# Kernel optimization log

Measured on AMD Instinct MI355X. Metric: run time of the kernel, lower is better.

Reference implementation:

```python
import jax, jax.numpy as jnp
import numpy as np

N, E = 20000, 640000
LATENT, HID, OUT, HEADS = 512, 256, 128, 2
NEG_SLOPE = 0.2


def setup_inputs() -> dict:
    key = jax.random.key(0)
    ks = jax.random.split(key, 12)
    s = 0.02
    return {
        "z": jax.random.normal(ks[0], (N, LATENT), dtype=jnp.float32),
        "edge_index": jax.random.randint(ks[1], (2, E), 0, N, dtype=jnp.int64),
        "W1": jax.random.normal(ks[2], (LATENT, HID), dtype=jnp.float32) * s,
        "b1": jnp.zeros((HID,), dtype=jnp.float32),
        "W2": jax.random.normal(ks[3], (HID, HID * HEADS), dtype=jnp.float32) * s,
        "b2": jnp.zeros((HID * HEADS,), dtype=jnp.float32),
        "Wg": jax.random.normal(ks[4], (HID * HEADS, HEADS * OUT), dtype=jnp.float32) * s,
        "att_src": jax.random.normal(ks[5], (HEADS, OUT), dtype=jnp.float32) * s,
        "att_dst": jax.random.normal(ks[6], (HEADS, OUT), dtype=jnp.float32) * s,
        "bias_g": jnp.zeros((HEADS * OUT,), dtype=jnp.float32),
        "W3": jax.random.normal(ks[7], (OUT * HEADS, 512), dtype=jnp.float32) * s,
        "b3": jnp.zeros((512,), dtype=jnp.float32),
    }


def _gat_conv(x, edge_index, Wg, att_src, att_dst, bias_g):
    n = x.shape[0]
    # add self loops (PyG GATConv default add_self_loops=True)
    loops = jnp.tile(jnp.arange(n, dtype=edge_index.dtype)[None, :], (2, 1))
    ei = jnp.concatenate([edge_index, loops], axis=1)
    src, dst = ei[0], ei[1]
    xp = (x @ Wg).reshape(n, HEADS, OUT)          # [N,H,C]
    a_src = jnp.einsum('nhc,hc->nh', xp, att_src)  # [N,H]
    a_dst = jnp.einsum('nhc,hc->nh', xp, att_dst)
    alpha = jax.nn.leaky_relu(a_src[src] + a_dst[dst], NEG_SLOPE)  # [E+N,H]
    amax = jax.ops.segment_max(alpha, dst, num_segments=n)
    alpha = jnp.exp(alpha - amax[dst])
    denom = jax.ops.segment_sum(alpha, dst, num_segments=n)
    alpha = alpha / jnp.maximum(denom[dst], 1e-16)
    msg = xp[src] * alpha[:, :, None]              # [E+N,H,C]
    out = jax.ops.segment_sum(msg, dst, num_segments=n)  # [N,H,C]
    return out.reshape(n, HEADS * OUT) + bias_g


def reference(z, edge_index, W1, b1, W2, b2, Wg, att_src, att_dst, bias_g, W3, b3):
    x = jax.nn.relu(z @ W1 + b1)
    x = jax.nn.relu(x @ W2 + b2)
    x = _gat_conv(x, edge_index, Wg, att_src, att_dst, bias_g)
    return x @ W3 + b3
```

## Files before the change

### kernel.cpp

```cpp
#include <hip/hip_runtime.h>
#include <hip/hip_bf16.h>
#include <float.h>

#define N_NODES 20000
#define LATENT  512
#define HID     256
#define OUT_C   128
#define HEADS   2
#define HC      256
#define NEG_SLOPE 0.2f

typedef _Float16 half8 __attribute__((ext_vector_type(8)));
typedef __attribute__((ext_vector_type(4))) float f32x4;

__device__ __forceinline__ ushort f2h(float v) {
    _Float16 h = (_Float16)v;
    return *(ushort*)&h;
}
__device__ __forceinline__ float h2f(ushort u) {
    _Float16 h = *(_Float16*)&u;
    return (float)h;
}

__device__ __forceinline__ void gl_lds16(const ushort* g, ushort* l) {
    __builtin_amdgcn_global_load_lds(
        (const __attribute__((address_space(1))) unsigned int*)g,
        (__attribute__((address_space(3))) unsigned int*)l, 16, 0, 0);
}

template<int BN>
__global__ __launch_bounds__(256) void gemm_f16(
    const ushort* __restrict__ A, const ushort* __restrict__ BT,
    const float* __restrict__ bias,
    float* __restrict__ Cf, ushort* __restrict__ Ch,
    int M, int N, int K, int relu)
{
    constexpr int NI  = BN / 32;
    constexpr int BUF = 4096 + BN * 32;
    __shared__ ushort lds[2 * BUF];
    ushort* buf0 = lds;
    ushort* buf1 = lds + BUF;

    const int t = threadIdx.x;
    const int l = t & 63;
    const int w = t >> 6;
    const int wm = (w >> 1) * 64;
    const int wn = (w & 1) * (BN / 2);
    const int lm = l & 15;
    const int q  = l >> 4;
    const int q4 = q * 4;

    const int row0 = blockIdx.x * 128;
    const int col0 = blockIdx.y * BN;

    const int jr0 = w * 16 + (l >> 2);
    const int gsh = (((l & 3) ^ ((l >> 4) & 3)) << 3);
    const ushort* gA0 = A + (size_t)(row0 + jr0) * K + gsh;
    const ushort* gA1 = gA0 + (size_t)64 * K;
    const ushort* gB0 = BT + (size_t)(col0 + jr0) * K + gsh;
    const ushort* gB1 = gB0 + (size_t)64 * K;
    const int dA0 = w * 512, dA1 = (4 + w) * 512;
    const int dB0 = 4096 + w * 512, dB1 = 4096 + (4 + w) * 512;

    const int csw = ((q ^ ((lm >> 2) & 3)) << 3);

    const f32x4 zf = {0.f, 0.f, 0.f, 0.f};
    f32x4 acc[4][NI];
    #pragma unroll
    for (int i = 0; i < 4; ++i)
        #pragma unroll
        for (int j = 0; j < NI; ++j) acc[i][j] = zf;

    auto issue = [&](int kk, ushort* B) {
        gl_lds16(gA0 + kk, B + dA0);
        gl_lds16(gA1 + kk, B + dA1);
        gl_lds16(gB0 + kk, B + dB0);
        if (BN == 128) gl_lds16(gB1 + kk, B + dB1);
    };

    auto compute = [&](const ushort* B) {
        half8 bf[NI];
        #pragma unroll
        for (int ni = 0; ni < NI; ++ni) {
            const int boff = (wn + ni * 16 + lm) * 32 + csw;
            bf[ni] = *(const half8*)&B[4096 + boff];
        }
        #pragma unroll
        for (int mi = 0; mi < 4; ++mi) {
            const int aoff = (wm + mi * 16 + lm) * 32 + csw;
            half8 af = *(const half8*)&B[aoff];
            #pragma unroll
            for (int ni = 0; ni < NI; ++ni)
                acc[mi][ni] = __builtin_amdgcn_mfma_f32_16x16x32_f16(
                    af, bf[ni], acc[mi][ni], 0, 0, 0);
        }
    };

    issue(0, buf0);
    __syncthreads();
    for (int k0 = 0; k0 < K; k0 += 64) {
        issue(k0 + 32, buf1);
        compute(buf0);
        __syncthreads();
        if (k0 + 64 < K) issue(k0 + 64, buf0);
        compute(buf1);
        __syncthreads();
    }

    #pragma unroll
    for (int mi = 0; mi < 4; ++mi) {
        #pragma unroll
        for (int ni = 0; ni < NI; ++ni) {
            const int col = col0 + wn + ni * 16 + lm;
            const float bv = bias ? bias[col] : 0.f;
            #pragma unroll
            for (int r = 0; r < 4; ++r) {
                const int row = row0 + wm + mi * 16 + q4 + r;
                if (row >= M) continue;
                float v = acc[mi][ni][r] + bv;
                if (relu) v = fmaxf(v, 0.f);
                const size_t idx = (size_t)row * N + col;
                if (Cf) Cf[idx] = v;
                if (Ch) Ch[idx] = f2h(v);
            }
        }
    }
}

__global__ __launch_bounds__(256) void cvt_kernel(
    const float* __restrict__ x, ushort* __restrict__ o, int n4)
{
    int i = blockIdx.x * 256 + threadIdx.x;
    if (i >= n4) return;
    float4 v = ((const float4*)x)[i];
    ((ushort4*)o)[i] = make_ushort4(f2h(v.x), f2h(v.y), f2h(v.z), f2h(v.w));
}

__global__ __launch_bounds__(256) void transpose_cvt_kernel(
    const float* __restrict__ W, ushort* __restrict__ T, int K, int N)
{
    int i = blockIdx.x * 256 + threadIdx.x;
    if (i >= K * N) return;
    int k = i / N, n = i - k * N;
    T[(size_t)n * K + k] = f2h(W[i]);
}

__global__ __launch_bounds__(256) void att_kernel(
    const ushort* __restrict__ xp, const float* __restrict__ att_src,
    const float* __restrict__ att_dst,
    float* __restrict__ a_src, float* __restrict__ a_dst, int n)
{
    int gw = (blockIdx.x * blockDim.x + threadIdx.x) >> 6;
    int lane = threadIdx.x & 63;
    if (gw >= 2 * n) return;
    int node = gw >> 1, h = gw & 1;
    const ushort* row = xp + (size_t)node * HC + h * OUT_C;
    const float* as = att_src + h * OUT_C;
    const float* ad = att_dst + h * OUT_C;
    float r0 = h2f(row[lane]), r1 = h2f(row[lane + 64]);
    float s1 = r0 * as[lane] + r1 * as[lane + 64];
    float s2 = r0 * ad[lane] + r1 * ad[lane + 64];
    #pragma unroll
    for (int off = 32; off > 0; off >>= 1) {
        s1 += __shfl_down(s1, off);
        s2 += __shfl_down(s2, off);
    }
    if (lane == 0) { a_src[gw] = s1; a_dst[gw] = s2; }
}

__global__ void zero_int2(int* deg, int* cursor, int n)
{
    int i = blockIdx.x * blockDim.x + threadIdx.x;
    if (i < n) { deg[i] = 0; cursor[i] = 0; }
}

__global__ __launch_bounds__(256) void hist_kernel(
    const int* __restrict__ dst, int* deg, int E_real, int ET)
{
    int e = blockIdx.x * blockDim.x + threadIdx.x;
    if (e >= ET) return;
    int d = (e < E_real) ? dst[e] : (e - E_real);
    atomicAdd(&deg[d], 1);
}

__global__ __launch_bounds__(256) void scan_kernel(
    const int* __restrict__ deg, int* __restrict__ rowptr, int n)
{
    __shared__ int part[256];
    const int t = threadIdx.x;
    const int chunk = (n + 255) / 256;
    const int lo = t * chunk;
    const int hi = min(lo + chunk, n);
    int s = 0;
    for (int i = lo; i < hi; ++i) s += deg[i];
    part[t] = s;
    __syncthreads();
    #pragma unroll
    for (int off = 1; off < 256; off <<= 1) {
        int add = (t >= off) ? part[t - off] : 0;
        __syncthreads();
        part[t] += add;
        __syncthreads();
    }
    int run = part[t] - s;
    for (int i = lo; i < hi; ++i) { rowptr[i] = run; run += deg[i]; }
    if (t == 255) rowptr[n] = part[255];
}

__global__ __launch_bounds__(256) void scatter_kernel(
    const int* __restrict__ src, const int* __restrict__ dst,
    const int* __restrict__ rowptr, int* cursor,
    int* __restrict__ sorted_src, int E_real, int ET)
{
    int e = blockIdx.x * blockDim.x + threadIdx.x;
    if (e >= ET) return;
    int s, d;
    if (e < E_real) { s = src[e]; d = dst[e]; }
    else            { s = e - E_real; d = s; }
    int pos = rowptr[d] + atomicAdd(&cursor[d], 1);
    sorted_src[pos] = s;
}

__global__ __launch_bounds__(64) void gat_aggregate(
    const int* __restrict__ rowptr, const int* __restrict__ sorted_src,
    const float* __restrict__ a_src, const float* __restrict__ a_dst,
    const ushort* __restrict__ xp, const float* __restrict__ bias_g,
    ushort* __restrict__ xg)
{
    __shared__ float s_w[2][64];
    __shared__ int   s_off[64];

    const int d = blockIdx.x;
    const int lane = threadIdx.x;
    const int h = lane >> 5;
    const int start = rowptr[d], end = rowptr[d + 1];

    const float ad0 = a_dst[2 * d + 0];
    const float ad1 = a_dst[2 * d + 1];

    float m0 = -FLT_MAX, m1 = -FLT_MAX;
    for (int e = start + lane; e < end; e += 64) {
        int s = sorted_src[e];
        float v0 = a_src[2 * s + 0] + ad0;
        float v1 = a_src[2 * s + 1] + ad1;
        v0 = (v0 > 0.f) ? v0 : NEG_SLOPE * v0;
        v1 = (v1 > 0.f) ? v1 : NEG_SLOPE * v1;
        m0 = fmaxf(m0, v0);
        m1 = fmaxf(m1, v1);
    }
    #pragma unroll
    for (int off = 32; off > 0; off >>= 1) {
        m0 = fmaxf(m0, __shfl_xor(m0, off));
        m1 = fmaxf(m1, __shfl_xor(m1, off));
    }

    float4 acc = make_float4(0.f, 0.f, 0.f, 0.f);
    float denom = 0.f;
    for (int e0 = start; e0 < end; e0 += 64) {
        int cnt = min(64, end - e0);
        if (lane < cnt) {
            int s = sorted_src[e0 + lane];
            float v0 = a_src[2 * s + 0] + ad0;
            float v1 = a_src[2 * s + 1] + ad1;
            v0 = (v0 > 0.f) ? v0 : NEG_SLOPE * v0;
            v1 = (v1 > 0.f) ? v1 : NEG_SLOPE * v1;
            s_w[0][lane] = expf(v0 - m0);
            s_w[1][lane] = expf(v1 - m1);
            s_off[lane] = s * HC;
        }
        __syncthreads();
        for (int j = 0; j < cnt; ++j) {
            float w = s_w[h][j];
            const ushort4 v = *(const ushort4*)(xp + s_off[j] + 4 * lane);
            denom += w;
            acc.x += w * h2f(v.x); acc.y += w * h2f(v.y);
            acc.z += w * h2f(v.z); acc.w += w * h2f(v.w);
        }
        __syncthreads();
    }

    float inv = 1.f / fmaxf(denom, 1e-16f);
    int c = 4 * lane;
    float4 bg = *(const float4*)(bias_g + c);
    const size_t base = ((size_t)d * HC + c) >> 2;
    ((ushort4*)xg)[base] = make_ushort4(
        f2h(acc.x * inv + bg.x), f2h(acc.y * inv + bg.y),
        f2h(acc.z * inv + bg.z), f2h(acc.w * inv + bg.w));
}

extern "C" void kernel_launch(void* const* d_in, const int* in_sizes, int n_in,
                              void* d_out, int out_size, void* d_ws, size_t ws_size,
                              hipStream_t stream)
{
    const float* z       = (const float*)d_in[0];
    const int*   ei      = (const int*)d_in[1];
    const float* W1      = (const float*)d_in[2];
    const float* b1      = (const float*)d_in[3];
    const float* W2      = (const float*)d_in[4];
    const float* b2      = (const float*)d_in[5];
    const float* Wg      = (const float*)d_in[6];
    const float* att_src = (const float*)d_in[7];
    const float* att_dst = (const float*)d_in[8];
    const float* bias_g  = (const float*)d_in[9];
    const float* W3      = (const float*)d_in[10];
    const float* b3      = (const float*)d_in[11];
    float* out = (float*)d_out;

    const int n = N_NODES;
    const int E_real = in_sizes[1] / 2;
    const int ET = E_real + n;
    const int* src = ei;
    const int* dst = ei + E_real;

    char* p = (char*)d_ws;
    auto alloc = [&](size_t bytes) {
        char* r = p;
        p += (bytes + 63) & ~(size_t)63;
        return r;
    };
    const int np = n + 128;
    ushort* z_f16  = (ushort*)alloc((size_t)np * LATENT * 2);
    ushort* x1_f16 = (ushort*)alloc((size_t)np * HID * 2);
    ushort* xp_f16 = (ushort*)alloc((size_t)n * HC * 2);
    ushort* W1T = (ushort*)alloc((size_t)LATENT * HID * 2);
    ushort* W2T = (ushort*)alloc((size_t)HID * 512 * 2);
    ushort* WgT = (ushort*)alloc((size_t)512 * HC * 2);
    ushort* W3T = (ushort*)alloc((size_t)HC * 512 * 2);
    float* a_src = (float*)alloc((size_t)2 * n * 4);
    float* a_dst = (float*)alloc((size_t)2 * n * 4);
    int* deg        = (int*)alloc((size_t)n * 4);
    int* rowptr     = (int*)alloc(((size_t)n + 1) * 4);
    int* cursor     = (int*)alloc((size_t)n * 4);
    int* sorted_src = (int*)alloc((size_t)ET * 4);
    ushort* x2_f16 = z_f16;
    ushort* xg_f16 = x1_f16;

    const int gm128 = (n + 127) / 128;

    cvt_kernel<<<(n * LATENT / 4 + 255) / 256, 256, 0, stream>>>(
        z, z_f16, n * LATENT / 4);
    transpose_cvt_kernel<<<(LATENT * HID + 255) / 256, 256, 0, stream>>>(
        W1, W1T, LATENT, HID);
    transpose_cvt_kernel<<<(HID * 512 + 255) / 256, 256, 0, stream>>>(
        W2, W2T, HID, 512);
    transpose_cvt_kernel<<<(512 * HC + 255) / 256, 256, 0, stream>>>(
        Wg, WgT, 512, HC);
    transpose_cvt_kernel<<<(HC * 512 + 255) / 256, 256, 0, stream>>>(
        W3, W3T, HC, 512);

    gemm_f16<64><<<dim3(gm128, HID / 64), 256, 0, stream>>>(
        z_f16, W1T, b1, nullptr, x1_f16, n, HID, LATENT, 1);
    gemm_f16<128><<<dim3(gm128, 512 / 128), 256, 0, stream>>>(
        x1_f16, W2T, b2, nullptr, x2_f16, n, 512, HID, 1);
    gemm_f16<64><<<dim3(gm128, HC / 64), 256, 0, stream>>>(
        x2_f16, WgT, nullptr, nullptr, xp_f16, n, HC, 512, 0);

    att_kernel<<<(2 * n + 3) / 4, 256, 0, stream>>>(
        xp_f16, att_src, att_dst, a_src, a_dst, n);
    zero_int2<<<(n + 255) / 256, 256, 0, stream>>>(deg, cursor, n);
    hist_kernel<<<(ET + 255) / 256, 256, 0, stream>>>(dst, deg, E_real, ET);
    scan_kernel<<<1, 256, 0, stream>>>(deg, rowptr, n);
    scatter_kernel<<<(ET + 255) / 256, 256, 0, stream>>>(
        src, dst, rowptr, cursor, sorted_src, E_real, ET);
    gat_aggregate<<<n, 64, 0, stream>>>(
        rowptr, sorted_src, a_src, a_dst, xp_f16, bias_g, xg_f16);

    gemm_f16<128><<<dim3(gm128, 512 / 128), 256, 0, stream>>>(
        xg_f16, W3T, b3, out, nullptr, n, 512, HC, 0);
}
```

Baseline: 350.9 us.

## Merge prep kernels, vectorize attention scores, use 64-wide GEMM tiles

```diff
diff --git a/kernel.cpp b/kernel.cpp
--- a/kernel.cpp
+++ b/kernel.cpp
@@ -127,20 +127,30 @@
     }
 }
 
-__global__ __launch_bounds__(256) void cvt_kernel(
-    const float* __restrict__ x, ushort* __restrict__ o, int n4)
+__global__ __launch_bounds__(256) void cvt_zero_kernel(
+    const float* __restrict__ x, ushort* __restrict__ o, int n4,
+    int* deg, int* cursor, int n)
 {
     int i = blockIdx.x * 256 + threadIdx.x;
+    if (i < n) { deg[i] = 0; cursor[i] = 0; }
     if (i >= n4) return;
     float4 v = ((const float4*)x)[i];
     ((ushort4*)o)[i] = make_ushort4(f2h(v.x), f2h(v.y), f2h(v.z), f2h(v.w));
 }
 
-__global__ __launch_bounds__(256) void transpose_cvt_kernel(
-    const float* __restrict__ W, ushort* __restrict__ T, int K, int N)
-{
-    int i = blockIdx.x * 256 + threadIdx.x;
-    if (i >= K * N) return;
+__global__ __launch_bounds__(256) void transpose_cvt4_kernel(
+    const float* __restrict__ W1, const float* __restrict__ W2,
+    const float* __restrict__ Wg, const float* __restrict__ W3,
+    ushort* __restrict__ T1, ushort* __restrict__ T2,
+    ushort* __restrict__ Tg, ushort* __restrict__ T3)
+{
+    int idx = blockIdx.x * 256 + threadIdx.x;
+    int which = idx >> 17, i = idx & 131071;
+    const float* W; ushort* T; int K, N;
+    if (which == 0)      { W = W1; T = T1; K = 512; N = 256; }
+    else if (which == 1) { W = W2; T = T2; K = 256; N = 512; }
+    else if (which == 2) { W = Wg; T = Tg; K = 512; N = 256; }
+    else                 { W = W3; T = T3; K = 256; N = 512; }
     int k = i / N, n = i - k * N;
     T[(size_t)n * K + k] = f2h(W[i]);
 }
@@ -150,28 +160,23 @@
     const float* __restrict__ att_dst,
     float* __restrict__ a_src, float* __restrict__ a_dst, int n)
 {
-    int gw = (blockIdx.x * blockDim.x + threadIdx.x) >> 6;
+    int node = (blockIdx.x * 256 + threadIdx.x) >> 6;
     int lane = threadIdx.x & 63;
-    if (gw >= 2 * n) return;
-    int node = gw >> 1, h = gw & 1;
-    const ushort* row = xp + (size_t)node * HC + h * OUT_C;
-    const float* as = att_src + h * OUT_C;
-    const float* ad = att_dst + h * OUT_C;
-    float r0 = h2f(row[lane]), r1 = h2f(row[lane + 64]);
-    float s1 = r0 * as[lane] + r1 * as[lane + 64];
-    float s2 = r0 * ad[lane] + r1 * ad[lane + 64];
-    #pragma unroll
-    for (int off = 32; off > 0; off >>= 1) {
-        s1 += __shfl_down(s1, off);
-        s2 += __shfl_down(s2, off);
-    }
-    if (lane == 0) { a_src[gw] = s1; a_dst[gw] = s2; }
-}
-
-__global__ void zero_int2(int* deg, int* cursor, int n)
-{
-    int i = blockIdx.x * blockDim.x + threadIdx.x;
-    if (i < n) { deg[i] = 0; cursor[i] = 0; }
+    if (node >= n) return;
+    int h = lane >> 5, lh = lane & 31;
+    int c = h * OUT_C + lh * 4;
+    const ushort4 v = *(const ushort4*)(xp + (size_t)node * HC + c);
+    const float4 as = *(const float4*)(att_src + c);
+    const float4 ad = *(const float4*)(att_dst + c);
+    float x0 = h2f(v.x), x1 = h2f(v.y), x2 = h2f(v.z), x3 = h2f(v.w);
+    float s1 = x0 * as.x + x1 * as.y + x2 * as.z + x3 * as.w;
+    float s2 = x0 * ad.x + x1 * ad.y + x2 * ad.z + x3 * ad.w;
+    #pragma unroll
+    for (int off = 16; off > 0; off >>= 1) {
+        s1 += __shfl_xor(s1, off);
+        s2 += __shfl_xor(s2, off);
+    }
+    if (lh == 0) { a_src[2 * node + h] = s1; a_dst[2 * node + h] = s2; }
 }
 
 __global__ __launch_bounds__(256) void hist_kernel(
@@ -337,27 +342,20 @@
 
     const int gm128 = (n + 127) / 128;
 
-    cvt_kernel<<<(n * LATENT / 4 + 255) / 256, 256, 0, stream>>>(
-        z, z_f16, n * LATENT / 4);
-    transpose_cvt_kernel<<<(LATENT * HID + 255) / 256, 256, 0, stream>>>(
-        W1, W1T, LATENT, HID);
-    transpose_cvt_kernel<<<(HID * 512 + 255) / 256, 256, 0, stream>>>(
-        W2, W2T, HID, 512);
-    transpose_cvt_kernel<<<(512 * HC + 255) / 256, 256, 0, stream>>>(
-        Wg, WgT, 512, HC);
-    transpose_cvt_kernel<<<(HC * 512 + 255) / 256, 256, 0, stream>>>(
-        W3, W3T, HC, 512);
+    cvt_zero_kernel<<<(n * LATENT / 4 + 255) / 256, 256, 0, stream>>>(
+        z, z_f16, n * LATENT / 4, deg, cursor, n);
+    transpose_cvt4_kernel<<<(4 * 131072) / 256, 256, 0, stream>>>(
+        W1, W2, Wg, W3, W1T, W2T, WgT, W3T);
 
     gemm_f16<64><<<dim3(gm128, HID / 64), 256, 0, stream>>>(
         z_f16, W1T, b1, nullptr, x1_f16, n, HID, LATENT, 1);
-    gemm_f16<128><<<dim3(gm128, 512 / 128), 256, 0, stream>>>(
+    gemm_f16<64><<<dim3(gm128, 512 / 64), 256, 0, stream>>>(
         x1_f16, W2T, b2, nullptr, x2_f16, n, 512, HID, 1);
     gemm_f16<64><<<dim3(gm128, HC / 64), 256, 0, stream>>>(
         x2_f16, WgT, nullptr, nullptr, xp_f16, n, HC, 512, 0);
 
-    att_kernel<<<(2 * n + 3) / 4, 256, 0, stream>>>(
+    att_kernel<<<(n * 64 + 255) / 256, 256, 0, stream>>>(
         xp_f16, att_src, att_dst, a_src, a_dst, n);
-    zero_int2<<<(n + 255) / 256, 256, 0, stream>>>(deg, cursor, n);
     hist_kernel<<<(ET + 255) / 256, 256, 0, stream>>>(dst, deg, E_real, ET);
     scan_kernel<<<1, 256, 0, stream>>>(deg, rowptr, n);
     scatter_kernel<<<(ET + 255) / 256, 256, 0, stream>>>(
@@ -365,6 +363,6 @@
     gat_aggregate<<<n, 64, 0, stream>>>(
         rowptr, sorted_src, a_src, a_dst, xp_f16, bias_g, xg_f16);
 
-    gemm_f16<128><<<dim3(gm128, 512 / 128), 256, 0, stream>>>(
+    gemm_f16<64><<<dim3(gm128, 512 / 64), 256, 0, stream>>>(
         xg_f16, W3T, b3, out, nullptr, n, 512, HC, 0);
 }
```

Measured after the change: 338.5 us. -3.5%, faster.
